# Optimization experiments

Hardware: AMD Instinct MI355X
Metric: run time of the kernel (lower is better)

Reference implementation:

```python
import math
import jax, jax.numpy as jnp
import numpy as np

N_FFT = 1024
HOP = 320
WIN = 800
SR = 32000
N_MELS = 128
FMIN = 0.0
FMAX = SR / 2.0
NUM_BINS = N_FFT // 2 + 1  # 513
PREEMPH = 0.97


def _hann_window(n):
    # torch.hann_window(n, periodic=False): 0.5 - 0.5*cos(2*pi*i/(n-1))
    i = np.arange(n, dtype=np.float64)
    return (0.5 - 0.5 * np.cos(2.0 * np.pi * i / (n - 1))).astype(np.float32)


def _fourier_basis():
    offset = (N_FFT - WIN) // 2
    win_full = np.zeros(N_FFT, dtype=np.float64)
    win_full[offset:offset + WIN] = _hann_window(WIN)
    n = np.arange(N_FFT, dtype=np.float64)[None, :]
    k = np.arange(NUM_BINS, dtype=np.float64)[:, None]
    ang = 2.0 * np.pi * k * (n / float(N_FFT))
    cos_k = np.cos(ang) * win_full
    sin_k = -np.sin(ang) * win_full
    return np.concatenate([cos_k, sin_k], axis=0).astype(np.float32)  # [2*513, 1024]


def _kaldi_mel_banks():
    # torchaudio.compliance.kaldi.get_mel_banks with vtln_warp_factor=1.0
    num_fft_bins = N_FFT // 2
    fft_bin_width = SR / float(N_FFT)
    mel = lambda f: 1127.0 * np.log(1.0 + f / 700.0)
    mel_low, mel_high = mel(FMIN), mel(FMAX)
    delta = (mel_high - mel_low) / (N_MELS + 1)
    left = mel_low + np.arange(N_MELS, dtype=np.float64) * delta  # [M]
    right = left + 2.0 * delta
    freqs = fft_bin_width * np.arange(num_fft_bins, dtype=np.float64)
    m = mel(freqs)[None, :]  # [1, 512]
    up = (m - left[:, None]) / delta
    down = (right[:, None] - m) / delta
    bank = np.maximum(0.0, np.minimum(up, down))  # [128, 512]
    bank = np.pad(bank, ((0, 0), (0, 1)))  # pad one zero column -> [128, 513]
    return bank.astype(np.float32)


def setup_inputs() -> dict:
    key = jax.random.key(0)
    x = jax.random.normal(key, (32, 320000), dtype=jnp.float32)
    return {
        "x": x,
        "fourier_basis": jnp.asarray(_fourier_basis()),
        "mel_basis": jnp.asarray(_kaldi_mel_banks()),
    }


def reference(x, fourier_basis, mel_basis):
    # preemphasis: conv1d with kernel [-0.97, 1.0] (cross-correlation)
    y = x[:, 1:] - PREEMPH * x[:, :-1]  # [B, T-1]
    # center pad by n_fft//2
    pad = N_FFT // 2
    y = jnp.pad(y, ((0, 0), (pad, pad)))
    Tp = y.shape[1]
    frames = (Tp - N_FFT) // HOP + 1
    # frame extraction: [B, frames, n_fft]
    idx = jnp.arange(frames)[:, None] * HOP + jnp.arange(N_FFT)[None, :]
    f = y[:, idx]
    # explicit DFT via dense matmul: [B, 2*num_bins, frames]
    spec = jnp.einsum('btn,cn->bct', f, fourier_basis)
    real = spec[:, :NUM_BINS, :]
    imag = spec[:, NUM_BINS:, :]
    power = real * real + imag * imag  # [B, num_bins, frames]
    mel = jnp.einsum('mf,bft->bmt', mel_basis, power)
    log_mel = (jnp.log(mel + 1e-05) + 4.5) / 5.0
    return log_mel
```

## Files before the change

kernel.cpp:

```cpp
#include <hip/hip_runtime.h>
#include <math.h>

typedef _Float16 half8 __attribute__((ext_vector_type(8)));
typedef float f32x4 __attribute__((ext_vector_type(4)));

constexpr int kNFFT    = 1024;
constexpr int kHop     = 320;
constexpr int kMels    = 128;
constexpr int kFrames  = 1000;
constexpr int kBatch   = 32;
constexpr int kXLen    = 320000;
constexpr int kYLen    = kXLen - 1;
constexpr int kYPad    = 328704;
constexpr int kYOff    = 512;
constexpr float kPre   = 0.97f;
constexpr int kPStride = 544;
constexpr int kKsLo    = 3;
constexpr int kKsHi    = 28;

constexpr size_t kYLvl     = (size_t)kBatch * kYPad;
constexpr size_t kFragLvl  = 64ull * 32 * 64 * 8;
constexpr size_t kFragOff  = 2 * kYLvl;
constexpr size_t kMelFrOff = kFragOff + 2 * kFragLvl;
constexpr size_t kMelFrSz  = 8ull * 17 * 64 * 8;
constexpr size_t kPowOff   = kMelFrOff + kMelFrSz;

constexpr int kYJobBlks   = (kYPad / 8 + 255) / 256;
constexpr int kYJobTotal  = kYJobBlks * kBatch;
constexpr int kFragBlks   = 131072 / 256;
constexpr int kMelBlks    = (8 * 17 * 64) / 256;
constexpr int kPrepGrid   = kYJobTotal + kFragBlks + kMelBlks;

__global__ void prep_all(const float* __restrict__ x, const float* __restrict__ basis,
                         const float* __restrict__ melb, _Float16* __restrict__ ws) {
    _Float16* ypad  = ws;
    _Float16* fr    = ws + kFragOff;
    _Float16* melfr = ws + kMelFrOff;
    const int bid = blockIdx.x;
    const int tid = threadIdx.x;

    if (bid < kYJobTotal) {
        int b = bid / kYJobBlks;
        int blk = bid - b * kYJobBlks;
        int e0 = (blk * 256 + tid) * 8;
        if (e0 >= kYPad) return;
        const float* xb = x + (size_t)b * kXLen;
        int yi = e0 - kYOff;
        float v[8];
        if (yi >= 0 && yi <= kXLen - 9) {
            float4 A = *(const float4*)(xb + yi);
            float4 B = *(const float4*)(xb + yi + 4);
            float C = xb[yi + 8];
            v[0] = A.y - kPre * A.x;  v[1] = A.z - kPre * A.y;
            v[2] = A.w - kPre * A.z;  v[3] = B.x - kPre * A.w;
            v[4] = B.y - kPre * B.x;  v[5] = B.z - kPre * B.y;
            v[6] = B.w - kPre * B.z;  v[7] = C   - kPre * B.w;
        } else {
            #pragma unroll
            for (int j = 0; j < 8; ++j) {
                int g = yi + j;
                v[j] = (g >= 0 && g < kYLen) ? xb[g + 1] - kPre * xb[g] : 0.0f;
            }
        }
        half8 hv, mv;
        #pragma unroll
        for (int j = 0; j < 8; ++j) {
            _Float16 h = (_Float16)v[j];
            hv[j] = h;
            mv[j] = (_Float16)(v[j] - (float)h);
        }
        size_t idx = (size_t)b * kYPad + e0;
        *(half8*)(ypad + idx) = hv;
        *(half8*)(ypad + idx + kYLvl) = mv;
    } else if (bid < kYJobTotal + kFragBlks) {
        int id = (bid - kYJobTotal) * 256 + tid;
        int L  = id & 63;
        int ks = (id >> 6) & 31;
        int g  = id >> 11;
        int r  = 16 * g + (L & 15);
        int orig = (r <= 512) ? r : r + 1;
        const float* src = basis + (size_t)orig * kNFFT + 32 * ks + (L >> 4) * 8;
        float4 s0 = *(const float4*)(src);
        float4 s1 = *(const float4*)(src + 4);
        float a[8] = {s0.x, s0.y, s0.z, s0.w, s1.x, s1.y, s1.z, s1.w};
        half8 hv, mv;
        #pragma unroll
        for (int j = 0; j < 8; ++j) {
            _Float16 h = (_Float16)a[j];
            hv[j] = h;
            mv[j] = (_Float16)(a[j] - (float)h);
        }
        _Float16* dst = fr + (size_t)id * 8;
        *(half8*)dst = hv;
        *(half8*)(dst + kFragLvl) = mv;
    } else {
        int id = (bid - kYJobTotal - kFragBlks) * 256 + tid;
        if (id >= 8 * 17 * 64) return;
        int f = id / 1088;
        int rem = id - f * 1088;
        int ks = rem >> 6;
        int L = rem & 63;
        int m = 16 * f + (L & 15);
        int kb = 32 * ks + (L >> 4) * 8;
        half8 hv;
        #pragma unroll
        for (int j = 0; j < 8; ++j) {
            int k = kb + j;
            hv[j] = (k < 513) ? (_Float16)melb[(size_t)m * 513 + k] : (_Float16)0.0f;
        }
        *(half8*)(melfr + (size_t)id * 8) = hv;
    }
}

__global__ __launch_bounds__(256, 2)
void stft_power(const _Float16* __restrict__ frags,
                const _Float16* __restrict__ ypad,
                _Float16* __restrict__ pw) {
    __shared__ __align__(16) _Float16 ash[2][16 * 512];
    const int tid  = threadIdx.x;
    const int w    = tid >> 6;
    const int lane = tid & 63;
    const int quad = lane >> 4;
    const int l16  = lane & 15;
    const int nt = blockIdx.x, g = blockIdx.y, b = blockIdx.z;
    const int t0 = nt * 256 + w * 64;
    const _Float16* yb0 = ypad + (size_t)b * kYPad;
    const _Float16* yb1 = yb0 + kYLvl;

    f32x4 acc[8][4] = {};

    auto stageA = [&](int ks, int pbuf) {
        #pragma unroll
        for (int c = 0; c < 4; ++c) {
            int slot = w + 4 * c;
            int f = slot & 7, lv = slot >> 3;
            int Gf = (f < 4) ? (4 * g + f) : (32 + 4 * g + (f - 4));
            const _Float16* gp = frags + (size_t)lv * kFragLvl
                               + ((size_t)(Gf * 32 + ks) * 64 + lane) * 8;
            __builtin_amdgcn_global_load_lds(
                (const __attribute__((address_space(1))) void*)gp,
                (__attribute__((address_space(3))) void*)&ash[pbuf][slot * 512],
                16, 0, 0);
        }
    };
    auto loadB2 = [&](int ks, int nf0, half8* bh, half8* bm) {
        #pragma unroll
        for (int nf = nf0; nf < nf0 + 2; ++nf) {
            int off = (t0 + nf * 16 + l16) * kHop + ks * 32 + quad * 8;
            bh[nf] = *(const half8*)(yb0 + off);
            bm[nf] = *(const half8*)(yb1 + off);
        }
    };
    auto mfma2 = [&](int f0, half8 h0, half8 m0, half8 h1, half8 m1,
                     half8* bh, half8* bm) {
        #pragma unroll
        for (int nf = 0; nf < 4; ++nf) {
            f32x4 a = acc[f0][nf];
            a = __builtin_amdgcn_mfma_f32_16x16x32_f16(h0, bh[nf], a, 0, 0, 0);
            a = __builtin_amdgcn_mfma_f32_16x16x32_f16(m0, bh[nf], a, 0, 0, 0);
            a = __builtin_amdgcn_mfma_f32_16x16x32_f16(h0, bm[nf], a, 0, 0, 0);
            acc[f0][nf] = a;
            f32x4 c = acc[f0 + 1][nf];
            c = __builtin_amdgcn_mfma_f32_16x16x32_f16(h1, bh[nf], c, 0, 0, 0);
            c = __builtin_amdgcn_mfma_f32_16x16x32_f16(m1, bh[nf], c, 0, 0, 0);
            c = __builtin_amdgcn_mfma_f32_16x16x32_f16(h1, bm[nf], c, 0, 0, 0);
            acc[f0 + 1][nf] = c;
        }
    };

    auto step = [&](int ks, int pbuf, half8* bhC, half8* bmC,
                    half8* bhN, half8* bmN, bool next) {
        #pragma unroll
        for (int p = 0; p < 4; ++p) {
            const int f0 = 2 * p;
            half8 h0 = *(const half8*)&ash[pbuf][f0 * 512 + lane * 8];
            half8 m0 = *(const half8*)&ash[pbuf][(8 + f0) * 512 + lane * 8];
            half8 h1 = *(const half8*)&ash[pbuf][(f0 + 1) * 512 + lane * 8];
            half8 m1 = *(const half8*)&ash[pbuf][(9 + f0) * 512 + lane * 8];
            if (p == 0 && next) stageA(ks + 1, pbuf ^ 1);
            if (p == 1 && next) loadB2(ks + 1, 0, bhN, bmN);
            if (p == 2 && next) loadB2(ks + 1, 2, bhN, bmN);
            if (p == 3)
                asm volatile("s_waitcnt vmcnt(8)" ::: "memory");
            __builtin_amdgcn_s_barrier();
            __builtin_amdgcn_s_setprio(1);
            mfma2(f0, h0, m0, h1, m1, bhC, bmC);
            __builtin_amdgcn_s_setprio(0);
            __builtin_amdgcn_s_barrier();
        }
    };

    half8 bhA[4], bmA[4], bhB[4], bmB[4];
    stageA(kKsLo, 0);
    loadB2(kKsLo, 0, bhA, bmA);
    loadB2(kKsLo, 2, bhA, bmA);
    asm volatile("s_waitcnt vmcnt(0)" ::: "memory");
    __builtin_amdgcn_s_barrier();

    for (int kss = 0; kss < 13; ++kss) {
        int ks = kKsLo + 2 * kss;
        step(ks,     0, bhA, bmA, bhB, bmB, true);
        step(ks + 1, 1, bhB, bmB, bhA, bmA, kss < 12);
    }

    #pragma unroll
    for (int mf = 0; mf < 4; ++mf) {
        int b0 = 64 * g + 16 * mf + 4 * quad;
        #pragma unroll
        for (int nf = 0; nf < 4; ++nf) {
            int t = t0 + nf * 16 + l16;
            size_t row = ((size_t)((b << 10) + t)) * kPStride;
            struct alignas(8) h4 { _Float16 v[4]; } pp;
            #pragma unroll
            for (int rr = 0; rr < 4; ++rr) {
                float pA = acc[mf][nf][rr];
                float pB = acc[4 + mf][nf][rr];
                float p2 = pA * pA + pB * pB;
                if (g == 0 && mf == 0 && quad == 0 && rr == 0) {
                    p2 = pA * pA;
                    pw[row + 512] = (_Float16)(pB * pB);
                }
                pp.v[rr] = (_Float16)p2;
            }
            *(decltype(pp)*)&pw[row + b0] = pp;
        }
    }
}

__global__ __launch_bounds__(256)
void mel_mfma(const _Float16* __restrict__ melfr, const _Float16* __restrict__ pw,
              float* __restrict__ out) {
    const int tid  = threadIdx.x;
    const int w    = tid >> 6;
    const int lane = tid & 63;
    const int quad = lane >> 4;
    const int l16  = lane & 15;
    const int nt = blockIdx.x, b = blockIdx.y;
    const int t = nt * 64 + w * 16 + l16;

    f32x4 acc[8] = {};
    for (int ks = 0; ks < 17; ++ks) {
        half8 bp = *(const half8*)(pw + ((size_t)((b << 10) + t)) * kPStride
                                   + 32 * ks + quad * 8);
        #pragma unroll
        for (int f = 0; f < 8; ++f) {
            half8 af = *(const half8*)(melfr + ((size_t)(f * 17 + ks) * 64 + lane) * 8);
            acc[f] = __builtin_amdgcn_mfma_f32_16x16x32_f16(af, bp, acc[f], 0, 0, 0);
        }
    }
    if (t < kFrames) {
        #pragma unroll
        for (int f = 0; f < 8; ++f) {
            #pragma unroll
            for (int r = 0; r < 4; ++r) {
                int m = 16 * f + 4 * quad + r;
                out[((size_t)(b * kMels + m)) * kFrames + t] =
                    (__logf(acc[f][r] + 1e-5f) + 4.5f) * 0.2f;
            }
        }
    }
}

extern "C" void kernel_launch(void* const* d_in, const int* in_sizes, int n_in,
                              void* d_out, int out_size, void* d_ws, size_t ws_size,
                              hipStream_t stream) {
    const float* x     = (const float*)d_in[0];
    const float* basis = (const float*)d_in[1];
    const float* melb  = (const float*)d_in[2];
    float* out = (float*)d_out;

    _Float16* ws    = (_Float16*)d_ws;
    _Float16* frags = ws + kFragOff;
    _Float16* melfr = ws + kMelFrOff;
    _Float16* pw    = ws + kPowOff;

    prep_all<<<dim3(kPrepGrid), 256, 0, stream>>>(x, basis, melb, ws);
    stft_power<<<dim3(4, 8, kBatch), 256, 0, stream>>>(frags, ws, pw);
    mel_mfma<<<dim3(16, kBatch), 256, 0, stream>>>(melfr, ws + kPowOff, out);
}
```

Baseline: 262.0 us.

## Switch STFT matmul from 16x16x32 to 32x32x16 MFMA tiles

Reorganizes the STFT power kernel to use 32x32x16 f16 MFMA instructions instead of 16x16x32, with the basis fragment layout, LDS staging slots, B-operand loads and output epilogue all remapped to the 32-row tile shape. The larger MFMA tile cuts the number of instructions and the operand register traffic for each unit of FLOPs, and it also changes the accumulator register footprint. The split-precision (hi/lo fp16) three-product scheme is kept, and the k-loop is split into two 16-wide halves per 32-wide step.

```diff
diff --git a/kernel.cpp b/kernel.cpp
--- a/kernel.cpp
+++ b/kernel.cpp
@@ -3,6 +3,7 @@
 
 typedef _Float16 half8 __attribute__((ext_vector_type(8)));
 typedef float f32x4 __attribute__((ext_vector_type(4)));
+typedef float f32x16 __attribute__((ext_vector_type(16)));
 
 constexpr int kNFFT    = 1024;
 constexpr int kHop     = 320;
@@ -74,12 +75,12 @@
         *(half8*)(ypad + idx + kYLvl) = mv;
     } else if (bid < kYJobTotal + kFragBlks) {
         int id = (bid - kYJobTotal) * 256 + tid;
-        int L  = id & 63;
-        int ks = (id >> 6) & 31;
-        int g  = id >> 11;
-        int r  = 16 * g + (L & 15);
+        int L    = id & 63;
+        int ksub = (id >> 6) & 63;
+        int G    = id >> 12;
+        int r    = 32 * G + (L & 31);
         int orig = (r <= 512) ? r : r + 1;
-        const float* src = basis + (size_t)orig * kNFFT + 32 * ks + (L >> 4) * 8;
+        const float* src = basis + (size_t)orig * kNFFT + 16 * ksub + (L >> 5) * 8;
         float4 s0 = *(const float4*)(src);
         float4 s1 = *(const float4*)(src + 4);
         float a[8] = {s0.x, s0.y, s0.z, s0.w, s1.x, s1.y, s1.z, s1.w};
@@ -120,80 +121,83 @@
     const int tid  = threadIdx.x;
     const int w    = tid >> 6;
     const int lane = tid & 63;
-    const int quad = lane >> 4;
-    const int l16  = lane & 15;
+    const int l32  = lane & 31;
+    const int hi   = lane >> 5;
     const int nt = blockIdx.x, g = blockIdx.y, b = blockIdx.z;
     const int t0 = nt * 256 + w * 64;
     const _Float16* yb0 = ypad + (size_t)b * kYPad;
     const _Float16* yb1 = yb0 + kYLvl;
 
-    f32x4 acc[8][4] = {};
+    f32x16 acc[4][2] = {};
 
     auto stageA = [&](int ks, int pbuf) {
         #pragma unroll
         for (int c = 0; c < 4; ++c) {
-            int slot = w + 4 * c;
-            int f = slot & 7, lv = slot >> 3;
-            int Gf = (f < 4) ? (4 * g + f) : (32 + 4 * g + (f - 4));
+            int s = w + 4 * c;
+            int lv = s >> 3, mt = (s >> 1) & 3, kl = s & 1;
+            int G = (mt < 2) ? (2 * g + mt) : (16 + 2 * g + (mt - 2));
             const _Float16* gp = frags + (size_t)lv * kFragLvl
-                               + ((size_t)(Gf * 32 + ks) * 64 + lane) * 8;
+                               + ((size_t)(G * 64 + 2 * ks + kl) * 64 + lane) * 8;
             __builtin_amdgcn_global_load_lds(
                 (const __attribute__((address_space(1))) void*)gp,
-                (__attribute__((address_space(3))) void*)&ash[pbuf][slot * 512],
+                (__attribute__((address_space(3))) void*)&ash[pbuf][s * 512],
                 16, 0, 0);
         }
     };
-    auto loadB2 = [&](int ks, int nf0, half8* bh, half8* bm) {
-        #pragma unroll
-        for (int nf = nf0; nf < nf0 + 2; ++nf) {
-            int off = (t0 + nf * 16 + l16) * kHop + ks * 32 + quad * 8;
-            bh[nf] = *(const half8*)(yb0 + off);
-            bm[nf] = *(const half8*)(yb1 + off);
+    auto loadB = [&](int ks, int kl, half8 (&bh)[2][2], half8 (&bm)[2][2]) {
+        #pragma unroll
+        for (int nf = 0; nf < 2; ++nf) {
+            int off = (t0 + nf * 32 + l32) * kHop + ks * 32 + kl * 16 + hi * 8;
+            bh[nf][kl] = *(const half8*)(yb0 + off);
+            bm[nf][kl] = *(const half8*)(yb1 + off);
         }
     };
-    auto mfma2 = [&](int f0, half8 h0, half8 m0, half8 h1, half8 m1,
-                     half8* bh, half8* bm) {
-        #pragma unroll
-        for (int nf = 0; nf < 4; ++nf) {
-            f32x4 a = acc[f0][nf];
-            a = __builtin_amdgcn_mfma_f32_16x16x32_f16(h0, bh[nf], a, 0, 0, 0);
-            a = __builtin_amdgcn_mfma_f32_16x16x32_f16(m0, bh[nf], a, 0, 0, 0);
-            a = __builtin_amdgcn_mfma_f32_16x16x32_f16(h0, bm[nf], a, 0, 0, 0);
-            acc[f0][nf] = a;
-            f32x4 c = acc[f0 + 1][nf];
-            c = __builtin_amdgcn_mfma_f32_16x16x32_f16(h1, bh[nf], c, 0, 0, 0);
-            c = __builtin_amdgcn_mfma_f32_16x16x32_f16(m1, bh[nf], c, 0, 0, 0);
-            c = __builtin_amdgcn_mfma_f32_16x16x32_f16(h1, bm[nf], c, 0, 0, 0);
-            acc[f0 + 1][nf] = c;
-        }
-    };
-
-    auto step = [&](int ks, int pbuf, half8* bhC, half8* bmC,
-                    half8* bhN, half8* bmN, bool next) {
-        #pragma unroll
-        for (int p = 0; p < 4; ++p) {
-            const int f0 = 2 * p;
-            half8 h0 = *(const half8*)&ash[pbuf][f0 * 512 + lane * 8];
-            half8 m0 = *(const half8*)&ash[pbuf][(8 + f0) * 512 + lane * 8];
-            half8 h1 = *(const half8*)&ash[pbuf][(f0 + 1) * 512 + lane * 8];
-            half8 m1 = *(const half8*)&ash[pbuf][(9 + f0) * 512 + lane * 8];
+
+    half8 bhA[2][2], bmA[2][2], bhB[2][2], bmB[2][2];
+
+    auto step = [&](int ks, int pbuf, half8 (&bhC)[2][2], half8 (&bmC)[2][2],
+                    half8 (&bhN)[2][2], half8 (&bmN)[2][2], bool next) {
+        #pragma unroll
+        for (int p = 0; p < 2; ++p) {
+            half8 a[2][2][2];
+            #pragma unroll
+            for (int mtl = 0; mtl < 2; ++mtl)
+                #pragma unroll
+                for (int lv = 0; lv < 2; ++lv)
+                    #pragma unroll
+                    for (int kl = 0; kl < 2; ++kl)
+                        a[mtl][lv][kl] = *(const half8*)
+                            &ash[pbuf][((lv << 3) | ((2 * p + mtl) << 1) | kl) * 512 + lane * 8];
             if (p == 0 && next) stageA(ks + 1, pbuf ^ 1);
-            if (p == 1 && next) loadB2(ks + 1, 0, bhN, bmN);
-            if (p == 2 && next) loadB2(ks + 1, 2, bhN, bmN);
-            if (p == 3)
+            if (p == 0 && next) loadB(ks + 1, 0, bhN, bmN);
+            if (p == 1 && next) {
+                loadB(ks + 1, 1, bhN, bmN);
                 asm volatile("s_waitcnt vmcnt(8)" ::: "memory");
+            }
             __builtin_amdgcn_s_barrier();
             __builtin_amdgcn_s_setprio(1);
-            mfma2(f0, h0, m0, h1, m1, bhC, bmC);
+            #pragma unroll
+            for (int mtl = 0; mtl < 2; ++mtl) {
+                #pragma unroll
+                for (int nf = 0; nf < 2; ++nf) {
+                    f32x16 c = acc[2 * p + mtl][nf];
+                    #pragma unroll
+                    for (int kl = 0; kl < 2; ++kl) {
+                        c = __builtin_amdgcn_mfma_f32_32x32x16_f16(a[mtl][0][kl], bhC[nf][kl], c, 0, 0, 0);
+                        c = __builtin_amdgcn_mfma_f32_32x32x16_f16(a[mtl][1][kl], bhC[nf][kl], c, 0, 0, 0);
+                        c = __builtin_amdgcn_mfma_f32_32x32x16_f16(a[mtl][0][kl], bmC[nf][kl], c, 0, 0, 0);
+                    }
+                    acc[2 * p + mtl][nf] = c;
+                }
+            }
             __builtin_amdgcn_s_setprio(0);
             __builtin_amdgcn_s_barrier();
         }
     };
 
-    half8 bhA[4], bmA[4], bhB[4], bmB[4];
     stageA(kKsLo, 0);
-    loadB2(kKsLo, 0, bhA, bmA);
-    loadB2(kKsLo, 2, bhA, bmA);
+    loadB(kKsLo, 0, bhA, bmA);
+    loadB(kKsLo, 1, bhA, bmA);
     asm volatile("s_waitcnt vmcnt(0)" ::: "memory");
     __builtin_amdgcn_s_barrier();
 
@@ -204,25 +208,31 @@
     }
 
     #pragma unroll
-    for (int mf = 0; mf < 4; ++mf) {
-        int b0 = 64 * g + 16 * mf + 4 * quad;
-        #pragma unroll
-        for (int nf = 0; nf < 4; ++nf) {
-            int t = t0 + nf * 16 + l16;
+    for (int mt = 0; mt < 2; ++mt) {
+        #pragma unroll
+        for (int nf = 0; nf < 2; ++nf) {
+            int t = t0 + nf * 32 + l32;
             size_t row = ((size_t)((b << 10) + t)) * kPStride;
-            struct alignas(8) h4 { _Float16 v[4]; } pp;
-            #pragma unroll
-            for (int rr = 0; rr < 4; ++rr) {
-                float pA = acc[mf][nf][rr];
-                float pB = acc[4 + mf][nf][rr];
-                float p2 = pA * pA + pB * pB;
-                if (g == 0 && mf == 0 && quad == 0 && rr == 0) {
-                    p2 = pA * pA;
-                    pw[row + 512] = (_Float16)(pB * pB);
+            int base = 64 * g + 32 * mt + 4 * hi;
+            #pragma unroll
+            for (int q = 0; q < 4; ++q) {
+                struct alignas(8) h4 { _Float16 v[4]; } pp;
+                #pragma unroll
+                for (int s = 0; s < 4; ++s) {
+                    int r = 4 * q + s;
+                    float pA = acc[mt][nf][r];
+                    float pB = acc[mt + 2][nf][r];
+                    float p2 = pA * pA + pB * pB;
+                    if (mt == 0 && q == 0 && s == 0) {
+                        if (g == 0 && hi == 0) {
+                            p2 = pA * pA;
+                            pw[row + 512] = (_Float16)(pB * pB);
+                        }
+                    }
+                    pp.v[s] = (_Float16)p2;
                 }
-                pp.v[rr] = (_Float16)p2;
-            }
-            *(decltype(pp)*)&pw[row + b0] = pp;
+                *(decltype(pp)*)&pw[row + base + 8 * q] = pp;
+            }
         }
     }
 }
```

Result: slower. 296.5 us (+13.1%).
